# Optimization experiments

Hardware: AMD Instinct MI355X
Metric: run time of the kernel (lower is better)

## Reference

```python
import jax, jax.numpy as jnp
import numpy as np


def setup_inputs() -> dict:
    key = jax.random.key(0)
    kK, kV, kQ = jax.random.split(key, 3)
    B, D, S = 4, 64, 4096
    K = jax.random.normal(kK, (B, D, S), dtype=jnp.float32)
    V = jax.random.normal(kV, (B, D, S), dtype=jnp.float32)
    Q = jax.random.normal(kQ, (B, D, S), dtype=jnp.float32)
    return {"K": K, "V": V, "Q": Q}


def reference(K, V, Q):
    # K,V: [B, D, Sk], Q: [B, D, Sq]
    d = Q.shape[1]
    # A[b,k,q] = sum_d K[b,d,k] * Q[b,d,q] / sqrt(d)
    A = jnp.einsum("bdk,bdq->bkq", K, Q) / jnp.sqrt(jnp.asarray(d, Q.dtype))
    A = jax.nn.softmax(A, axis=1)  # normalize over keys (dim 1), matching F.softmax(A, 1)
    # R[b,d,q] = sum_k V[b,d,k] * A[b,k,q]
    R = jnp.einsum("bdk,bkq->bdq", V, A)
    return jnp.concatenate((R, Q), axis=1)  # [B, 2D, Sq]
```

## Files before the change

### kernel.cpp

```cpp
#include <hip/hip_runtime.h>
#include <hip/hip_bf16.h>

#define S_LEN 4096
#define D_DIM 64
#define QB 64
#define KB 32
#define NT (S_LEN / KB)
#define TILE_E 4096

typedef __attribute__((ext_vector_type(8)))  short bf16x8;
typedef __attribute__((ext_vector_type(16))) float f32x16;
typedef unsigned int u32;

#define Z16 {0.f,0.f,0.f,0.f,0.f,0.f,0.f,0.f,0.f,0.f,0.f,0.f,0.f,0.f,0.f,0.f}

union bpack8 { __hip_bfloat16 h[8]; bf16x8 v; };
union ppack  { u32 w[4]; bf16x8 v; };

static __device__ __forceinline__ float fexp2(float x) {
    return __builtin_amdgcn_exp2f(x);
}
static __device__ __forceinline__ u32 cvtpk(float lo, float hi) {
    u32 r;
    asm("v_cvt_pk_bf16_f32 %0, %1, %2" : "=v"(r) : "v"(lo), "v"(hi));
    return r;
}
static __device__ __forceinline__ void plswap(u32 &a, u32 &b) {
    asm("v_permlane32_swap_b32 %0, %1" : "+v"(a), "+v"(b));
}

struct pfrag { ppack p0, p1; };
static __device__ __forceinline__ pfrag packP(const f32x16& s) {
    u32 A = cvtpk(s[0],  s[1]),  Bw = cvtpk(s[2],  s[3]);
    u32 C = cvtpk(s[4],  s[5]),  Dw = cvtpk(s[6],  s[7]);
    u32 E = cvtpk(s[8],  s[9]),  F  = cvtpk(s[10], s[11]);
    u32 G = cvtpk(s[12], s[13]), H  = cvtpk(s[14], s[15]);
    plswap(A, C); plswap(Bw, Dw); plswap(E, G); plswap(F, H);
    pfrag r;
    r.p0.w[0] = A; r.p0.w[1] = Bw; r.p0.w[2] = C; r.p0.w[3] = Dw;
    r.p1.w[0] = E; r.p1.w[1] = F;  r.p1.w[2] = G; r.p1.w[3] = H;
    return r;
}
static __device__ __forceinline__ float treesum(const f32x16& s) {
    float a0 = (s[0] + s[1])   + (s[2] + s[3]);
    float a1 = (s[4] + s[5])   + (s[6] + s[7]);
    float a2 = (s[8] + s[9])   + (s[10] + s[11]);
    float a3 = (s[12] + s[13]) + (s[14] + s[15]);
    return (a0 + a1) + (a2 + a3);
}

#define GLD16(gp, lp) __builtin_amdgcn_global_load_lds( \
    (const __attribute__((address_space(1))) u32*)(const void*)(gp), \
    (__attribute__((address_space(3))) u32*)(void*)(lp), 16, 0, 0)

#define QSCALE 0.18033688011112042f

__global__ __launch_bounds__(256)
void prep_kv(const float* __restrict__ K, const float* __restrict__ V,
             __hip_bfloat16* __restrict__ KVbf)
{
    const int b = blockIdx.y, x = blockIdx.x, z = blockIdx.z;
    const int t = threadIdx.x;

    if (z == 0) {
        const int key = t & 31, dg = t >> 5;
        const float* src = K + ((size_t)b * D_DIM + dg * 8) * S_LEN + x * KB + key;
        bpack8 u;
        #pragma unroll
        for (int e = 0; e < 8; ++e)
            u.h[e] = __float2bfloat16(src[(size_t)e * S_LEN]);
        *(bf16x8*)&KVbf[((size_t)b * NT + x) * TILE_E + t * 8] = u.v;
    } else {
        const int d = t >> 2, kg = t & 3;
        const float* p = V + ((size_t)b * D_DIM + d) * S_LEN + x * KB + kg * 8;
        float4 a = *(const float4*)p, c = *(const float4*)(p + 4);
        bpack8 u;
        u.h[0] = __float2bfloat16(a.x); u.h[1] = __float2bfloat16(a.y);
        u.h[2] = __float2bfloat16(a.z); u.h[3] = __float2bfloat16(a.w);
        u.h[4] = __float2bfloat16(c.x); u.h[5] = __float2bfloat16(c.y);
        u.h[6] = __float2bfloat16(c.z); u.h[7] = __float2bfloat16(c.w);
        *(bf16x8*)&KVbf[((size_t)b * NT + x) * TILE_E + 2048 + (kg * 64 + d) * 8] = u.v;
    }
}

__global__ __launch_bounds__(512, 2)
void attn_fwd(const __hip_bfloat16* __restrict__ KVbf,
              const float* __restrict__ Qg,
              float* __restrict__ out)
{
    const int b  = blockIdx.y;
    const int q0 = blockIdx.x * QB;
    const int t  = threadIdx.x;
    const int lane = t & 63;
    const int w    = t >> 6;
    const int l5   = lane & 31;
    const int h    = lane >> 5;

    __shared__ __align__(16) char Ls[131072];
    char* myL = Ls + w * 16384;

    const int WT = NT / 8;
    const __hip_bfloat16* kvb = KVbf + ((size_t)b * NT + w * WT) * TILE_E;
    const float* Qblk = Qg + (size_t)b * D_DIM * S_LEN + q0;

    {
        float* QF = (float*)Ls;
        #pragma unroll
        for (int i = 0; i < 8; ++i) {
            int d = i * 8 + w;
            QF[d * 65 + lane] = Qblk[(size_t)d * S_LEN + lane] * QSCALE;
        }
        __syncthreads();
    }
    bf16x8 qfA[4], qfB[4];
    {
        const float* QF = (const float*)Ls;
        #pragma unroll
        for (int j = 0; j < 4; ++j) {
            float a[8], bq[8];
            #pragma unroll
            for (int e = 0; e < 8; ++e) {
                int dabs = (2 * j + h) * 8 + e;
                a[e]  = QF[dabs * 65 + l5];
                bq[e] = QF[dabs * 65 + 32 + l5];
            }
            ppack pa, pb;
            #pragma unroll
            for (int k2 = 0; k2 < 4; ++k2) {
                pa.w[k2] = cvtpk(a[2 * k2],  a[2 * k2 + 1]);
                pb.w[k2] = cvtpk(bq[2 * k2], bq[2 * k2 + 1]);
            }
            qfA[j] = pa.v;
            qfB[j] = pb.v;
        }
        __syncthreads();
    }

    #pragma unroll
    for (int i = 0; i < 8; ++i)
        GLD16(kvb + i * 512 + lane * 8, myL + i * 1024);
    asm volatile("s_waitcnt vmcnt(0)" ::: "memory");
    __builtin_amdgcn_sched_barrier(0);

    float lsumA = 0.f, lsumB = 0.f;
    f32x16 accA[2] = {Z16, Z16}, accB[2] = {Z16, Z16};
    int cur = 0;

    for (int it = 0; it < WT; ++it) {
        if (it + 1 < WT) {
            const __hip_bfloat16* nx = kvb + (size_t)(it + 1) * TILE_E;
            #pragma unroll
            for (int i = 0; i < 8; ++i)
                GLD16(nx + i * 512 + lane * 8, myL + (cur ^ 1) * 8192 + i * 1024);
        }
        const char* Lk = myL + cur * 8192;
        const char* Lv = Lk + 4096;

        bf16x8 kf[4];
        #pragma unroll
        for (int j = 0; j < 4; ++j)
            kf[j] = *(const bf16x8*)(Lk + ((2 * j + h) * 32 + l5) * 16);

        f32x16 sA = Z16, sB = Z16;
        __builtin_amdgcn_s_setprio(1);
        #pragma unroll
        for (int j = 0; j < 4; ++j) {
            sA = __builtin_amdgcn_mfma_f32_32x32x16_bf16(kf[j], qfA[j], sA, 0, 0, 0);
            sB = __builtin_amdgcn_mfma_f32_32x32x16_bf16(kf[j], qfB[j], sB, 0, 0, 0);
        }
        __builtin_amdgcn_s_setprio(0);

        bf16x8 vf[4];
        #pragma unroll
        for (int j = 0; j < 2; ++j)
            #pragma unroll
            for (int dt = 0; dt < 2; ++dt)
                vf[2 * j + dt] = *(const bf16x8*)(Lv + ((2 * j + h) * 64 + dt * 32 + l5) * 16);

        #pragma unroll
        for (int r = 0; r < 16; ++r) sA[r] = fexp2(sA[r]);
        #pragma unroll
        for (int r = 0; r < 16; ++r) sB[r] = fexp2(sB[r]);
        lsumA += treesum(sA);
        lsumB += treesum(sB);

        pfrag pA = packP(sA), pB = packP(sB);

        __builtin_amdgcn_s_setprio(1);
        #pragma unroll
        for (int j = 0; j < 2; ++j)
            #pragma unroll
            for (int dt = 0; dt < 2; ++dt) {
                const bf16x8 vv = vf[2 * j + dt];
                const ppack& pa = j ? pA.p1 : pA.p0;
                const ppack& pb = j ? pB.p1 : pB.p0;
                accA[dt] = __builtin_amdgcn_mfma_f32_32x32x16_bf16(vv, pa.v, accA[dt], 0, 0, 0);
                accB[dt] = __builtin_amdgcn_mfma_f32_32x32x16_bf16(vv, pb.v, accB[dt], 0, 0, 0);
            }
        __builtin_amdgcn_s_setprio(0);

        asm volatile("s_waitcnt vmcnt(0)" ::: "memory");
        __builtin_amdgcn_sched_barrier(0);
        cur ^= 1;
    }

    lsumA += __shfl_xor(lsumA, 32);
    lsumB += __shfl_xor(lsumB, 32);

    float* LF = (float*)Ls;
    __syncthreads();
    if (h == 0) {
        LF[w * 64 + l5]      = lsumA;
        LF[w * 64 + 32 + l5] = lsumB;
    }
    __syncthreads();
    const int qp = t & 63;
    float den = 0.f;
    #pragma unroll
    for (int w2 = 0; w2 < 8; ++w2) den += LF[w2 * 64 + qp];
    const float inv = 1.f / den;
    __syncthreads();

    #pragma unroll
    for (int dt = 0; dt < 2; ++dt)
        #pragma unroll
        for (int r = 0; r < 16; ++r) {
            int d = dt * 32 + (r & 3) + 8 * (r >> 2) + 4 * h;
            LF[w * 2048 + d * 32 + l5]         = accA[dt][r];
            LF[16384 + w * 2048 + d * 32 + l5] = accB[dt][r];
        }
    __syncthreads();

    const int dgrp = t >> 6;
    const int slab = (qp < 32) ? 0 : 16384;
    const int qs   = qp & 31;
    float* op = out + (size_t)b * 2 * D_DIM * S_LEN + q0 + qp;
    #pragma unroll
    for (int dd = 0; dd < 8; ++dd) {
        int d = dgrp * 8 + dd;
        float sum = 0.f;
        #pragma unroll
        for (int w2 = 0; w2 < 8; ++w2)
            sum += LF[slab + w2 * 2048 + d * 32 + qs];
        op[(size_t)d * S_LEN] = sum * inv;
    }

    {
        float* oq = out + ((size_t)b * 2 * D_DIM + D_DIM) * S_LEN + q0;
        #pragma unroll
        for (int i = 0; i < 8; ++i) {
            int d = i * 8 + w;
            oq[(size_t)d * S_LEN + lane] = Qblk[(size_t)d * S_LEN + lane];
        }
    }
}

extern "C" void kernel_launch(void* const* d_in, const int* in_sizes, int n_in,
                              void* d_out, int out_size, void* d_ws, size_t ws_size,
                              hipStream_t stream) {
    const float* K = (const float*)d_in[0];
    const float* V = (const float*)d_in[1];
    const float* Q = (const float*)d_in[2];
    float* out = (float*)d_out;

    const int B = in_sizes[0] / (D_DIM * S_LEN);
    __hip_bfloat16* KVbf = (__hip_bfloat16*)d_ws;

    prep_kv<<<dim3(NT, B, 2), dim3(256), 0, stream>>>(K, V, KVbf);

    attn_fwd<<<dim3(S_LEN / QB, B), dim3(512), 0, stream>>>(KVbf, Q, out);
}
```

Before: 34.42 us.

## Fuse KV bf16 prep into attention kernel with grid barrier; deepen prefetch

Folds the separate K/V bf16 conversion kernel into the attention kernel. Each block converts a slice of K/V, then all blocks meet at a global atomic spin barrier, which removes one kernel launch and its gap at the cost of a memset and the barrier. The KV tile loop also changes from a single-buffered next-tile prefetch to issuing loads two tiles ahead with partial vmcnt waits. The barrier depends on all 256 blocks being co-resident and gives up after a bounded spin, so correctness relies on occupancy.

Measured after the change: 58.20 us. 1.69x slower.

```diff
diff --git a/kernel.cpp b/kernel.cpp
--- a/kernel.cpp
+++ b/kernel.cpp
@@ -7,6 +7,7 @@
 #define KB 32
 #define NT (S_LEN / KB)
 #define TILE_E 4096
+#define WT (NT / 8)
 
 typedef __attribute__((ext_vector_type(8)))  short bf16x8;
 typedef __attribute__((ext_vector_type(16))) float f32x16;
@@ -84,13 +85,15 @@
 }
 
 __global__ __launch_bounds__(512, 2)
-void attn_fwd(const __hip_bfloat16* __restrict__ KVbf,
-              const float* __restrict__ Qg,
-              float* __restrict__ out)
+void attn_fused(const float* __restrict__ Kg, const float* __restrict__ Vg,
+                const float* __restrict__ Qg, float* __restrict__ out,
+                __hip_bfloat16* __restrict__ KVbf, unsigned* __restrict__ bar,
+                int do_prep)
 {
-    const int b  = blockIdx.y;
-    const int q0 = blockIdx.x * QB;
-    const int t  = threadIdx.x;
+    const int t   = threadIdx.x;
+    const int blk = blockIdx.x;
+    const int b   = blk >> 6;
+    const int q0  = (blk & 63) * QB;
     const int lane = t & 63;
     const int w    = t >> 6;
     const int l5   = lane & 31;
@@ -99,7 +102,49 @@
     __shared__ __align__(16) char Ls[131072];
     char* myL = Ls + w * 16384;
 
-    const int WT = NT / 8;
+    if (do_prep) {
+        const int gid = blk * 512 + t;
+        const int pb  = gid >> 15;
+        const int rem = gid & 32767;
+        const int x   = rem >> 8;
+        const int t8  = rem & 255;
+        {
+            const int key = t8 & 31, dg = t8 >> 5;
+            const float* src = Kg + ((size_t)pb * D_DIM + dg * 8) * S_LEN + x * KB + key;
+            bpack8 u;
+            #pragma unroll
+            for (int e = 0; e < 8; ++e)
+                u.h[e] = __float2bfloat16(src[(size_t)e * S_LEN]);
+            *(bf16x8*)&KVbf[((size_t)pb * NT + x) * TILE_E + t8 * 8] = u.v;
+        }
+        {
+            const int d = t8 >> 2, kg = t8 & 3;
+            const float* p = Vg + ((size_t)pb * D_DIM + d) * S_LEN + x * KB + kg * 8;
+            float4 a = *(const float4*)p, c = *(const float4*)(p + 4);
+            bpack8 u;
+            u.h[0] = __float2bfloat16(a.x); u.h[1] = __float2bfloat16(a.y);
+            u.h[2] = __float2bfloat16(a.z); u.h[3] = __float2bfloat16(a.w);
+            u.h[4] = __float2bfloat16(c.x); u.h[5] = __float2bfloat16(c.y);
+            u.h[6] = __float2bfloat16(c.z); u.h[7] = __float2bfloat16(c.w);
+            *(bf16x8*)&KVbf[((size_t)pb * NT + x) * TILE_E + 2048 + (kg * 64 + d) * 8] = u.v;
+        }
+        __syncthreads();
+        if (t == 0) {
+            __threadfence();
+            unsigned arrived = atomicAdd(bar, 1u) + 1u;
+            if (arrived == (unsigned)gridDim.x) {
+                atomicExch(bar + 1, 1u);
+            } else {
+                for (int spin = 0; spin < (1 << 16); ++spin) {
+                    if (atomicAdd(bar + 1, 0u) != 0u) break;
+                    __builtin_amdgcn_s_sleep(16);
+                }
+            }
+            __threadfence();
+        }
+        __syncthreads();
+    }
+
     const __hip_bfloat16* kvb = KVbf + ((size_t)b * NT + w * WT) * TILE_E;
     const float* Qblk = Qg + (size_t)b * D_DIM * S_LEN + q0;
 
@@ -138,28 +183,31 @@
 
     #pragma unroll
     for (int i = 0; i < 8; ++i)
-        GLD16(kvb + i * 512 + lane * 8, myL + i * 1024);
-    asm volatile("s_waitcnt vmcnt(0)" ::: "memory");
-    __builtin_amdgcn_sched_barrier(0);
+        GLD16(kvb + i * 512 + lane * 8,          myL + i * 1024);
+    #pragma unroll
+    for (int i = 0; i < 8; ++i)
+        GLD16(kvb + TILE_E + i * 512 + lane * 8, myL + 8192 + i * 1024);
 
     float lsumA = 0.f, lsumB = 0.f;
     f32x16 accA[2] = {Z16, Z16}, accB[2] = {Z16, Z16};
-    int cur = 0;
 
     for (int it = 0; it < WT; ++it) {
-        if (it + 1 < WT) {
-            const __hip_bfloat16* nx = kvb + (size_t)(it + 1) * TILE_E;
-            #pragma unroll
-            for (int i = 0; i < 8; ++i)
-                GLD16(nx + i * 512 + lane * 8, myL + (cur ^ 1) * 8192 + i * 1024);
-        }
-        const char* Lk = myL + cur * 8192;
+        if (it + 1 < WT) asm volatile("s_waitcnt vmcnt(8)" ::: "memory");
+        else             asm volatile("s_waitcnt vmcnt(0)" ::: "memory");
+        __builtin_amdgcn_sched_barrier(0);
+
+        const char* Lk = myL + (it & 1) * 8192;
         const char* Lv = Lk + 4096;
 
-        bf16x8 kf[4];
+        bf16x8 kf[4], vf[4];
         #pragma unroll
         for (int j = 0; j < 4; ++j)
             kf[j] = *(const bf16x8*)(Lk + ((2 * j + h) * 32 + l5) * 16);
+        #pragma unroll
+        for (int j = 0; j < 2; ++j)
+            #pragma unroll
+            for (int dt = 0; dt < 2; ++dt)
+                vf[2 * j + dt] = *(const bf16x8*)(Lv + ((2 * j + h) * 64 + dt * 32 + l5) * 16);
 
         f32x16 sA = Z16, sB = Z16;
         __builtin_amdgcn_s_setprio(1);
@@ -170,12 +218,14 @@
         }
         __builtin_amdgcn_s_setprio(0);
 
-        bf16x8 vf[4];
-        #pragma unroll
-        for (int j = 0; j < 2; ++j)
-            #pragma unroll
-            for (int dt = 0; dt < 2; ++dt)
-                vf[2 * j + dt] = *(const bf16x8*)(Lv + ((2 * j + h) * 64 + dt * 32 + l5) * 16);
+        if (it + 2 < WT) {
+            asm volatile("s_waitcnt lgkmcnt(0)" ::: "memory");
+            __builtin_amdgcn_sched_barrier(0);
+            const __hip_bfloat16* nx = kvb + (size_t)(it + 2) * TILE_E;
+            #pragma unroll
+            for (int i = 0; i < 8; ++i)
+                GLD16(nx + i * 512 + lane * 8, myL + (it & 1) * 8192 + i * 1024);
+        }
 
         #pragma unroll
         for (int r = 0; r < 16; ++r) sA[r] = fexp2(sA[r]);
@@ -198,10 +248,6 @@
                 accB[dt] = __builtin_amdgcn_mfma_f32_32x32x16_bf16(vv, pb.v, accB[dt], 0, 0, 0);
             }
         __builtin_amdgcn_s_setprio(0);
-
-        asm volatile("s_waitcnt vmcnt(0)" ::: "memory");
-        __builtin_amdgcn_sched_barrier(0);
-        cur ^= 1;
     }
 
     lsumA += __shfl_xor(lsumA, 32);
@@ -264,9 +310,15 @@
     float* out = (float*)d_out;
 
     const int B = in_sizes[0] / (D_DIM * S_LEN);
-    __hip_bfloat16* KVbf = (__hip_bfloat16*)d_ws;
-
-    prep_kv<<<dim3(NT, B, 2), dim3(256), 0, stream>>>(K, V, KVbf);
-
-    attn_fwd<<<dim3(S_LEN / QB, B), dim3(512), 0, stream>>>(KVbf, Q, out);
-}
+
+    unsigned* bar = (unsigned*)d_ws;
+    __hip_bfloat16* KVbf = (__hip_bfloat16*)((char*)d_ws + 256);
+
+    if (B == 4) {
+        hipMemsetAsync(bar, 0, 2 * sizeof(unsigned), stream);
+        attn_fused<<<dim3(256), dim3(512), 0, stream>>>(K, V, Q, out, KVbf, bar, 1);
+    } else {
+        prep_kv<<<dim3(NT, B, 2), dim3(256), 0, stream>>>(K, V, KVbf);
+        attn_fused<<<dim3(B * 64), dim3(512), 0, stream>>>(K, V, Q, out, KVbf, bar, 0);
+    }
+}
```

## Split key dimension across blocks with bf16 partials and separate combine kernel

Applied to the files above, without the earlier changes.

The attention kernel now uses 256-thread blocks, each covering a quarter of the keys (grid z=4). Every wave streams 8 KV tiles through single-buffered LDS, refilling K and V separately with fine-grained vmcnt waits. Partial numerators are reduced in LDS, written as bf16 to workspace along with partial denominators, then summed and normalized by a new combine kernel. The Q passthrough copy moves into the prep kernel. This raises occupancy and block count, at the cost of an extra launch, extra global traffic for the partials, and bf16 rounding of partial sums.

New measurement: 101.7 us. 2.96x slower.

```diff
diff --git a/kernel.cpp b/kernel.cpp
--- a/kernel.cpp
+++ b/kernel.cpp
@@ -3,10 +3,10 @@
 
 #define S_LEN 4096
 #define D_DIM 64
-#define QB 64
 #define KB 32
 #define NT (S_LEN / KB)
 #define TILE_E 4096
+#define WT2 8
 
 typedef __attribute__((ext_vector_type(8)))  short bf16x8;
 typedef __attribute__((ext_vector_type(16))) float f32x16;
@@ -16,6 +16,7 @@
 
 union bpack8 { __hip_bfloat16 h[8]; bf16x8 v; };
 union ppack  { u32 w[4]; bf16x8 v; };
+union bload4 { uint2 u; __hip_bfloat16 h[4]; };
 
 static __device__ __forceinline__ float fexp2(float x) {
     return __builtin_amdgcn_exp2f(x);
@@ -56,8 +57,9 @@
 #define QSCALE 0.18033688011112042f
 
 __global__ __launch_bounds__(256)
-void prep_kv(const float* __restrict__ K, const float* __restrict__ V,
-             __hip_bfloat16* __restrict__ KVbf)
+void prep_all(const float* __restrict__ K, const float* __restrict__ V,
+              const float* __restrict__ Q,
+              __hip_bfloat16* __restrict__ KVbf, float* __restrict__ out)
 {
     const int b = blockIdx.y, x = blockIdx.x, z = blockIdx.z;
     const int t = threadIdx.x;
@@ -70,7 +72,7 @@
         for (int e = 0; e < 8; ++e)
             u.h[e] = __float2bfloat16(src[(size_t)e * S_LEN]);
         *(bf16x8*)&KVbf[((size_t)b * NT + x) * TILE_E + t * 8] = u.v;
-    } else {
+    } else if (z == 1) {
         const int d = t >> 2, kg = t & 3;
         const float* p = V + ((size_t)b * D_DIM + d) * S_LEN + x * KB + kg * 8;
         float4 a = *(const float4*)p, c = *(const float4*)(p + 4);
@@ -80,34 +82,47 @@
         u.h[4] = __float2bfloat16(c.x); u.h[5] = __float2bfloat16(c.y);
         u.h[6] = __float2bfloat16(c.z); u.h[7] = __float2bfloat16(c.w);
         *(bf16x8*)&KVbf[((size_t)b * NT + x) * TILE_E + 2048 + (kg * 64 + d) * 8] = u.v;
-    }
-}
-
-__global__ __launch_bounds__(512, 2)
+    } else {
+        const int s0 = x * 32;
+        int idx = t;
+        #pragma unroll
+        for (int i = 0; i < 2; ++i, idx += 256) {
+            int d = idx >> 3, s4 = idx & 7;
+            float4 v = *(const float4*)&Q[((size_t)b * D_DIM + d) * S_LEN + s0 + s4 * 4];
+            *(float4*)&out[((size_t)b * 2 * D_DIM + D_DIM + d) * S_LEN + s0 + s4 * 4] = v;
+        }
+    }
+}
+
+__global__ __launch_bounds__(256, 4)
 void attn_fwd(const __hip_bfloat16* __restrict__ KVbf,
               const float* __restrict__ Qg,
-              float* __restrict__ out)
+              __hip_bfloat16* __restrict__ accPb, float* __restrict__ lP,
+              int nb)
 {
+    const int qb = blockIdx.x;
     const int b  = blockIdx.y;
-    const int q0 = blockIdx.x * QB;
+    const int kz = blockIdx.z;
+    const int q0 = qb * 64;
+
     const int t  = threadIdx.x;
     const int lane = t & 63;
     const int w    = t >> 6;
     const int l5   = lane & 31;
     const int h    = lane >> 5;
 
-    __shared__ __align__(16) char Ls[131072];
-    char* myL = Ls + w * 16384;
-
-    const int WT = NT / 8;
-    const __hip_bfloat16* kvb = KVbf + ((size_t)b * NT + w * WT) * TILE_E;
+    __shared__ __align__(16) char Ls[33792];
+    char* myK = Ls + w * 8192;
+    char* myV = myK + 4096;
+
+    const __hip_bfloat16* kvb = KVbf + ((size_t)b * NT + kz * 32 + w * WT2) * TILE_E;
     const float* Qblk = Qg + (size_t)b * D_DIM * S_LEN + q0;
 
     {
         float* QF = (float*)Ls;
         #pragma unroll
-        for (int i = 0; i < 8; ++i) {
-            int d = i * 8 + w;
+        for (int i = 0; i < 16; ++i) {
+            int d = i * 4 + w;
             QF[d * 65 + lane] = Qblk[(size_t)d * S_LEN + lane] * QSCALE;
         }
         __syncthreads();
@@ -137,29 +152,33 @@
     }
 
     #pragma unroll
-    for (int i = 0; i < 8; ++i)
-        GLD16(kvb + i * 512 + lane * 8, myL + i * 1024);
-    asm volatile("s_waitcnt vmcnt(0)" ::: "memory");
-    __builtin_amdgcn_sched_barrier(0);
+    for (int i = 0; i < 4; ++i)
+        GLD16(kvb + i * 512 + lane * 8,        myK + i * 1024);
+    #pragma unroll
+    for (int i = 0; i < 4; ++i)
+        GLD16(kvb + 2048 + i * 512 + lane * 8, myV + i * 1024);
 
     float lsumA = 0.f, lsumB = 0.f;
     f32x16 accA[2] = {Z16, Z16}, accB[2] = {Z16, Z16};
-    int cur = 0;
-
-    for (int it = 0; it < WT; ++it) {
-        if (it + 1 < WT) {
-            const __hip_bfloat16* nx = kvb + (size_t)(it + 1) * TILE_E;
-            #pragma unroll
-            for (int i = 0; i < 8; ++i)
-                GLD16(nx + i * 512 + lane * 8, myL + (cur ^ 1) * 8192 + i * 1024);
-        }
-        const char* Lk = myL + cur * 8192;
-        const char* Lv = Lk + 4096;
+
+    #pragma unroll
+    for (int it = 0; it < WT2; ++it) {
+        const __hip_bfloat16* nx = kvb + (size_t)(it + 1) * TILE_E;
+
+        asm volatile("s_waitcnt vmcnt(4)" ::: "memory");
+        __builtin_amdgcn_sched_barrier(0);
 
         bf16x8 kf[4];
         #pragma unroll
         for (int j = 0; j < 4; ++j)
-            kf[j] = *(const bf16x8*)(Lk + ((2 * j + h) * 32 + l5) * 16);
+            kf[j] = *(const bf16x8*)(myK + ((2 * j + h) * 32 + l5) * 16);
+        asm volatile("s_waitcnt lgkmcnt(0)" ::: "memory");
+        __builtin_amdgcn_sched_barrier(0);
+        if (it + 1 < WT2) {
+            #pragma unroll
+            for (int i = 0; i < 4; ++i)
+                GLD16(nx + i * 512 + lane * 8, myK + i * 1024);
+        }
 
         f32x16 sA = Z16, sB = Z16;
         __builtin_amdgcn_s_setprio(1);
@@ -170,12 +189,23 @@
         }
         __builtin_amdgcn_s_setprio(0);
 
+        if (it + 1 < WT2) { asm volatile("s_waitcnt vmcnt(4)" ::: "memory"); }
+        else              { asm volatile("s_waitcnt vmcnt(0)" ::: "memory"); }
+        __builtin_amdgcn_sched_barrier(0);
+
         bf16x8 vf[4];
         #pragma unroll
         for (int j = 0; j < 2; ++j)
             #pragma unroll
             for (int dt = 0; dt < 2; ++dt)
-                vf[2 * j + dt] = *(const bf16x8*)(Lv + ((2 * j + h) * 64 + dt * 32 + l5) * 16);
+                vf[2 * j + dt] = *(const bf16x8*)(myV + ((2 * j + h) * 64 + dt * 32 + l5) * 16);
+        asm volatile("s_waitcnt lgkmcnt(0)" ::: "memory");
+        __builtin_amdgcn_sched_barrier(0);
+        if (it + 1 < WT2) {
+            #pragma unroll
+            for (int i = 0; i < 4; ++i)
+                GLD16(nx + 2048 + i * 512 + lane * 8, myV + i * 1024);
+        }
 
         #pragma unroll
         for (int r = 0; r < 16; ++r) sA[r] = fexp2(sA[r]);
@@ -198,61 +228,99 @@
                 accB[dt] = __builtin_amdgcn_mfma_f32_32x32x16_bf16(vv, pb.v, accB[dt], 0, 0, 0);
             }
         __builtin_amdgcn_s_setprio(0);
-
-        asm volatile("s_waitcnt vmcnt(0)" ::: "memory");
-        __builtin_amdgcn_sched_barrier(0);
-        cur ^= 1;
     }
 
     lsumA += __shfl_xor(lsumA, 32);
     lsumB += __shfl_xor(lsumB, 32);
 
     float* LF = (float*)Ls;
+    float* LS = (float*)(Ls + 32768);
     __syncthreads();
+
     if (h == 0) {
-        LF[w * 64 + l5]      = lsumA;
-        LF[w * 64 + 32 + l5] = lsumB;
+        LS[w * 64 + l5]      = lsumA;
+        LS[w * 64 + 32 + l5] = lsumB;
+    }
+    if (w >= 2) {
+        float* slab = LF + (w - 2) * 4096;
+        #pragma unroll
+        for (int dt = 0; dt < 2; ++dt)
+            #pragma unroll
+            for (int r = 0; r < 16; ++r) {
+                int d = dt * 32 + (r & 3) + 8 * (r >> 2) + 4 * h;
+                slab[d * 64 + l5]      = accA[dt][r];
+                slab[d * 64 + 32 + l5] = accB[dt][r];
+            }
     }
     __syncthreads();
-    const int qp = t & 63;
-    float den = 0.f;
-    #pragma unroll
-    for (int w2 = 0; w2 < 8; ++w2) den += LF[w2 * 64 + qp];
-    const float inv = 1.f / den;
+    if (w < 2) {
+        const float* slab = LF + w * 4096;
+        #pragma unroll
+        for (int dt = 0; dt < 2; ++dt)
+            #pragma unroll
+            for (int r = 0; r < 16; ++r) {
+                int d = dt * 32 + (r & 3) + 8 * (r >> 2) + 4 * h;
+                accA[dt][r] += slab[d * 64 + l5];
+                accB[dt][r] += slab[d * 64 + 32 + l5];
+            }
+    }
     __syncthreads();
-
-    #pragma unroll
-    for (int dt = 0; dt < 2; ++dt)
-        #pragma unroll
-        for (int r = 0; r < 16; ++r) {
-            int d = dt * 32 + (r & 3) + 8 * (r >> 2) + 4 * h;
-            LF[w * 2048 + d * 32 + l5]         = accA[dt][r];
-            LF[16384 + w * 2048 + d * 32 + l5] = accB[dt][r];
-        }
+    if (w == 1) {
+        #pragma unroll
+        for (int dt = 0; dt < 2; ++dt)
+            #pragma unroll
+            for (int r = 0; r < 16; ++r) {
+                int d = dt * 32 + (r & 3) + 8 * (r >> 2) + 4 * h;
+                LF[d * 64 + l5]      = accA[dt][r];
+                LF[d * 64 + 32 + l5] = accB[dt][r];
+            }
+    }
     __syncthreads();
-
-    const int dgrp = t >> 6;
-    const int slab = (qp < 32) ? 0 : 16384;
-    const int qs   = qp & 31;
-    float* op = out + (size_t)b * 2 * D_DIM * S_LEN + q0 + qp;
-    #pragma unroll
-    for (int dd = 0; dd < 8; ++dd) {
-        int d = dgrp * 8 + dd;
-        float sum = 0.f;
-        #pragma unroll
-        for (int w2 = 0; w2 < 8; ++w2)
-            sum += LF[slab + w2 * 2048 + d * 32 + qs];
-        op[(size_t)d * S_LEN] = sum * inv;
-    }
-
-    {
-        float* oq = out + ((size_t)b * 2 * D_DIM + D_DIM) * S_LEN + q0;
-        #pragma unroll
-        for (int i = 0; i < 8; ++i) {
-            int d = i * 8 + w;
-            oq[(size_t)d * S_LEN + lane] = Qblk[(size_t)d * S_LEN + lane];
-        }
-    }
+    if (w == 0) {
+        __hip_bfloat16* ap = accPb + (size_t)(kz * nb + b) * D_DIM * S_LEN;
+        #pragma unroll
+        for (int dt = 0; dt < 2; ++dt)
+            #pragma unroll
+            for (int r = 0; r < 16; ++r) {
+                int d = dt * 32 + (r & 3) + 8 * (r >> 2) + 4 * h;
+                ap[(size_t)d * S_LEN + q0 + l5]      = __float2bfloat16(accA[dt][r] + LF[d * 64 + l5]);
+                ap[(size_t)d * S_LEN + q0 + 32 + l5] = __float2bfloat16(accB[dt][r] + LF[d * 64 + 32 + l5]);
+            }
+        if (h == 0) {
+            float dA = LS[l5]      + LS[64 + l5]      + LS[128 + l5]      + LS[192 + l5];
+            float dB = LS[32 + l5] + LS[64 + 32 + l5] + LS[128 + 32 + l5] + LS[192 + 32 + l5];
+            lP[(size_t)(kz * nb + b) * S_LEN + q0 + l5]      = dA;
+            lP[(size_t)(kz * nb + b) * S_LEN + q0 + 32 + l5] = dB;
+        }
+    }
+}
+
+__global__ __launch_bounds__(256)
+void attn_combine(const __hip_bfloat16* __restrict__ accPb,
+                  const float* __restrict__ lP,
+                  float* __restrict__ out, int nsplit, int nb)
+{
+    int gid = blockIdx.x * 256 + threadIdx.x;
+    int q4   = gid & (S_LEN / 4 - 1);
+    int rest = gid >> 10;
+    int d    = rest & (D_DIM - 1);
+    int b    = rest >> 6;
+    if (b >= nb) return;
+    size_t qoff = (size_t)q4 * 4;
+
+    float num[4] = {0.f,0.f,0.f,0.f}, den[4] = {0.f,0.f,0.f,0.f};
+    for (int z = 0; z < nsplit; ++z) {
+        bload4 a;
+        a.u = *(const uint2*)&accPb[((size_t)(z * nb + b) * D_DIM + d) * S_LEN + qoff];
+        float4 lz = *(const float4*)&lP[(size_t)(z * nb + b) * S_LEN + qoff];
+        num[0] += __bfloat162float(a.h[0]); num[1] += __bfloat162float(a.h[1]);
+        num[2] += __bfloat162float(a.h[2]); num[3] += __bfloat162float(a.h[3]);
+        den[0] += lz.x; den[1] += lz.y; den[2] += lz.z; den[3] += lz.w;
+    }
+    float4 r;
+    r.x = num[0] / den[0]; r.y = num[1] / den[1];
+    r.z = num[2] / den[2]; r.w = num[3] / den[3];
+    *(float4*)&out[((size_t)b * 2 * D_DIM + d) * S_LEN + qoff] = r;
 }
 
 extern "C" void kernel_launch(void* const* d_in, const int* in_sizes, int n_in,
@@ -264,9 +332,17 @@
     float* out = (float*)d_out;
 
     const int B = in_sizes[0] / (D_DIM * S_LEN);
-    __hip_bfloat16* KVbf = (__hip_bfloat16*)d_ws;
-
-    prep_kv<<<dim3(NT, B, 2), dim3(256), 0, stream>>>(K, V, KVbf);
-
-    attn_fwd<<<dim3(S_LEN / QB, B), dim3(512), 0, stream>>>(KVbf, Q, out);
-}
+    const size_t kvE = (size_t)B * NT * TILE_E;
+
+    __hip_bfloat16* KVbf  = (__hip_bfloat16*)d_ws;
+    __hip_bfloat16* accPb = KVbf + kvE;
+    float* lP = (float*)(accPb + (size_t)4 * B * D_DIM * S_LEN);
+
+    prep_all<<<dim3(NT, B, 3), dim3(256), 0, stream>>>(K, V, Q, KVbf, out);
+
+    attn_fwd<<<dim3(S_LEN / 64, B, 4), dim3(256), 0, stream>>>(
+        KVbf, Q, accPb, lP, B);
+
+    attn_combine<<<dim3(B * D_DIM * (S_LEN / 4) / 256), dim3(256), 0, stream>>>(
+        accPb, lP, out, 4, B);
+}
```
